# Kernel tuning notes

Hardware: AMD Instinct MI355X
Metric: run time of the kernel (lower is better)

## Reference

```python
import jax, jax.numpy as jnp
import numpy as np

B, S, H, NH, L = 8, 768, 768, 12, 12
W = 128          # one-sided window = attention_window // 2 (chunk_size=256)
D = H // NH      # head dim = 64
FF = 4 * H
EPS = 1e-12      # LongformerConfig layer_norm_eps
MAX_POS = 1024


def setup_inputs() -> dict:
    key = jax.random.key(0)
    ks = iter(jax.random.split(key, 64))
    rn = lambda shape, s=0.02: jax.random.normal(next(ks), shape, jnp.float32) * s
    inp = {
        "embedding": jax.random.normal(next(ks), (B, S, H), jnp.float32),
        "mask": jnp.ones((B, S), jnp.int32),  # unused by the original forward's core call
        "pos_emb": rn((MAX_POS, H)),
        "tte": rn((H,)),  # token_type embedding row 0 (token_type_ids are all zero)
        "emb_ln_g": jnp.ones((H,), jnp.float32),
        "emb_ln_b": jnp.zeros((H,), jnp.float32),
        "Wq": rn((L, H, H)), "bq": jnp.zeros((L, H), jnp.float32),
        "Wk": rn((L, H, H)), "bk": jnp.zeros((L, H), jnp.float32),
        "Wv": rn((L, H, H)), "bv": jnp.zeros((L, H), jnp.float32),
        "Wo": rn((L, H, H)), "bo": jnp.zeros((L, H), jnp.float32),
        "ln1_g": jnp.ones((L, H), jnp.float32), "ln1_b": jnp.zeros((L, H), jnp.float32),
        "Wi": rn((L, H, FF)), "bi": jnp.zeros((L, FF), jnp.float32),
        "Wo2": rn((L, FF, H)), "bo2": jnp.zeros((L, H), jnp.float32),
        "ln2_g": jnp.ones((L, H), jnp.float32), "ln2_b": jnp.zeros((L, H), jnp.float32),
        "gate_w": rn((H,)), "gate_b": jnp.zeros((), jnp.float32),
    }
    return inp


def layer_norm(x, g, b):
    mu = jnp.mean(x, axis=-1, keepdims=True)
    var = jnp.mean(jnp.square(x - mu), axis=-1, keepdims=True)
    return (x - mu) * jax.lax.rsqrt(var + EPS) * g + b


def sliding_window_attention(q, k, v):
    # q,k,v: [B,S,H]; each query attends to keys within +-W positions (band of 2W+1).
    n = S // W
    split = lambda x: x.reshape(B, S, NH, D).transpose(0, 2, 1, 3)  # [B,NH,S,D]
    qh = split(q) / np.sqrt(D)
    kh, vh = split(k), split(v)
    qc = qh.reshape(B, NH, n, W, D)

    def chunk3(x):
        # pad one chunk of zeros each side, gather [prev, cur, next] key chunks
        xp = jnp.pad(x, ((0, 0), (0, 0), (W, W), (0, 0))).reshape(B, NH, n + 2, W, D)
        return jnp.concatenate([xp[:, :, i:i + n] for i in range(3)], axis=3)  # [B,NH,n,3W,D]

    k3, v3 = chunk3(kh), chunk3(vh)
    scores = jnp.einsum('bhnqd,bhnkd->bhnqk', qc, k3)  # [B,NH,n,W,3W]

    qi = jnp.arange(W)[:, None]
    kj = jnp.arange(3 * W)[None, :]
    rel = kj - W - qi                                   # relative position j - i
    jglob = (jnp.arange(n)[:, None, None] - 1) * W + kj  # absolute key position
    valid = (jnp.abs(rel) <= W) & (jglob >= 0) & (jglob < S)  # [n,W,3W]

    scores = jnp.where(valid, scores, -1e9)
    p = jax.nn.softmax(scores, axis=-1)
    out = jnp.einsum('bhnqk,bhnkd->bhnqd', p, v3)
    return out.reshape(B, NH, S, D).transpose(0, 2, 1, 3).reshape(B, S, H)


def reference(embedding, mask, pos_emb, tte, emb_ln_g, emb_ln_b,
              Wq, bq, Wk, bk, Wv, bv, Wo, bo, ln1_g, ln1_b,
              Wi, bi, Wo2, bo2, ln2_g, ln2_b, gate_w, gate_b):
    # embeddings (position ids start at padding_idx+1 = 2, RoBERTa-style)
    pos_ids = jnp.arange(S) + 2
    x = embedding + pos_emb[pos_ids] + tte
    x = layer_norm(x, emb_ln_g, emb_ln_b)

    def layer(h, p):
        wq, b_q, wk, b_k, wv, b_v, wo, b_o, g1, be1, wi, b_i, wo2, b_o2, g2, be2 = p
        q = h @ wq + b_q
        k = h @ wk + b_k
        v = h @ wv + b_v
        a = sliding_window_attention(q, k, v)
        h = layer_norm(h + a @ wo + b_o, g1, be1)
        ff = jax.nn.gelu(h @ wi + b_i, approximate=False)
        h = layer_norm(h + ff @ wo2 + b_o2, g2, be2)
        return h, None

    x, _ = jax.lax.scan(layer, x, (Wq, bq, Wk, bk, Wv, bv, Wo, bo, ln1_g, ln1_b,
                                   Wi, bi, Wo2, bo2, ln2_g, ln2_b))
    gate = x @ gate_w + gate_b  # [B,S]
    return x, gate
```

## Files before the change

kernel.cpp:

```cpp
#include <hip/hip_runtime.h>
#include <hip/hip_bf16.h>
#include <math.h>
#include <stdint.h>

typedef __hip_bfloat16 bf16;
typedef __attribute__((ext_vector_type(8))) __bf16 bf16x8;
typedef __attribute__((ext_vector_type(4))) float f32x4;

#define HDIM 768
#define MROWS 6144
#define NCHUNK 6

__device__ __forceinline__ float bf2f(unsigned int u) {
  union { unsigned int i; float f; } c; c.i = u << 16; return c.f;
}

__device__ __forceinline__ void gload16(const void* g, void* l) {
  __builtin_amdgcn_global_load_lds((const __attribute__((address_space(1))) void*)g,
                                   (__attribute__((address_space(3))) void*)l, 16, 0, 0);
}

__device__ __forceinline__ float gelu_f(float v) {
  const float u2 = 1.5957691216057308f * (v + 0.044715f * v * v * v);
  const float e = __expf(u2);
  const float th = 1.f - 2.f / (e + 1.f);
  return 0.5f * v * (1.f + th);
}

__global__ __launch_bounds__(256) void wconv(
    const float* __restrict__ Wq, const float* __restrict__ Wk,
    const float* __restrict__ Wv, const float* __restrict__ Wo,
    const float* __restrict__ Wi, const float* __restrict__ Wo2,
    bf16* __restrict__ wt)
{
  __shared__ float tile[32][33];
  const int bid = blockIdx.x;
  const float* src; bf16* dst; int K, N, tIdx;
  if (bid < 2304) {
    int m = bid / 576; tIdx = bid % 576; K = 768; N = 768;
    src = (m == 0) ? Wq : (m == 1) ? Wk : (m == 2) ? Wv : Wo;
    dst = wt + (size_t)m * 589824;
  } else if (bid < 4608) {
    tIdx = bid - 2304; K = 768; N = 3072; src = Wi; dst = wt + 2359296;
  } else {
    tIdx = bid - 4608; K = 3072; N = 768; src = Wo2; dst = wt + 4718592;
  }
  const int tilesN = N >> 5;
  const int tn = tIdx % tilesN, tk = tIdx / tilesN;
  const int n0 = tn * 32, k0 = tk * 32;
  const int tx = threadIdx.x & 31, ty = threadIdx.x >> 5;
#pragma unroll
  for (int r = 0; r < 4; ++r)
    tile[ty + r * 8][tx] = src[(size_t)(k0 + ty + r * 8) * N + n0 + tx];
  __syncthreads();
#pragma unroll
  for (int r = 0; r < 4; ++r)
    dst[(size_t)(n0 + ty + r * 8) * K + k0 + tx] = __float2bfloat16(tile[tx][ty + r * 8]);
}

__global__ __launch_bounds__(512, 2) void gemm256(
    const bf16* __restrict__ A, const bf16* __restrict__ Bt,
    void* __restrict__ out, const float* __restrict__ b0,
    const float* __restrict__ b1, const float* __restrict__ b2,
    int gx, int N, int K, int NT, int epi)
{
  __shared__ __align__(16) bf16 As[2][2][8192];
  __shared__ __align__(16) bf16 Bs[2][2][8192];

  const int nwg = gridDim.x;
  const int wg = blockIdx.x;
  const int L = (wg & 7) * (nwg >> 3) + (wg >> 3);
  const int bx = L % gx, by = L / gx;
  const int m0 = by * 256, n0 = bx * 256;

  const int t = threadIdx.x;
  const int lane = t & 63;
  const int w = t >> 6;
  const int wr = w >> 2;
  const int wc = w & 3;
  const int fr = lane & 15;
  const int g = lane >> 4;

  f32x4 acc[8][4];
#pragma unroll
  for (int i = 0; i < 8; ++i)
#pragma unroll
    for (int j = 0; j < 4; ++j) acc[i][j] = (f32x4)0.f;

  const int r0 = t >> 2, q0 = t & 3;
  const int sq0 = q0 ^ ((r0 >> 1) & 3);
  const bf16* gA0 = A + (size_t)(m0 + r0) * K + sq0 * 8;
  const bf16* gB0 = Bt + (size_t)(n0 + r0) * K + sq0 * 8;
  const int dst0 = t * 16;

  unsigned offA[8], offB[4];
#pragma unroll
  for (int mf = 0; mf < 8; ++mf) {
    const int R = wr * 128 + mf * 16 + fr;
    offA[mf] = (unsigned)((R * 64 + g * 16) ^ (((R >> 1) & 3) << 4));
  }
#pragma unroll
  for (int nf = 0; nf < 4; ++nf) {
    const int R = wc * 64 + nf * 16 + fr;
    offB[nf] = (unsigned)((R * 64 + g * 16) ^ (((R >> 1) & 3) << 4));
  }
  const unsigned ldsA = (unsigned)(uintptr_t)&As[0][0][0];
  const unsigned ldsB = (unsigned)(uintptr_t)&Bs[0][0][0];

#define STAGE(KT, DB, KH) {                                                \
    const bf16* a_ = gA0 + (size_t)(KT) * 64 + (KH) * 32;                  \
    const bf16* b_ = gB0 + (size_t)(KT) * 64 + (KH) * 32;                  \
    gload16(a_, (char*)As[DB][KH] + dst0);                                 \
    gload16(a_ + (size_t)128 * K, (char*)As[DB][KH] + dst0 + 8192);        \
    gload16(b_, (char*)Bs[DB][KH] + dst0);                                 \
    gload16(b_ + (size_t)128 * K, (char*)Bs[DB][KH] + dst0 + 8192); }

  STAGE(0, 0, 0)
  STAGE(0, 0, 1)
  asm volatile("s_waitcnt vmcnt(4)" ::: "memory");
  __builtin_amdgcn_s_barrier();

#define PHASE(KT, KH, DB) {                                                \
    bf16x8 af[8], bfr[4];                                                  \
    const unsigned baA_ = ldsA + (DB) * 32768u + (KH) * 16384u;            \
    const unsigned baB_ = ldsB + (DB) * 32768u + (KH) * 16384u;            \
    _Pragma("unroll")                                                      \
    for (int mf = 0; mf < 8; ++mf)                                         \
      asm volatile("ds_read_b128 %0, %1" : "=v"(af[mf]) : "v"(baA_ + offA[mf])); \
    _Pragma("unroll")                                                      \
    for (int nf = 0; nf < 4; ++nf)                                         \
      asm volatile("ds_read_b128 %0, %1" : "=v"(bfr[nf]) : "v"(baB_ + offB[nf])); \
    const int pf_ = ((KT) + 1 < NT) ? (KT) + 1 : (KT);                     \
    STAGE(pf_, (DB) ^ 1, KH)                                               \
    asm volatile("s_waitcnt lgkmcnt(0)" ::: "memory");                     \
    __builtin_amdgcn_sched_barrier(0);                                     \
    __builtin_amdgcn_s_setprio(1);                                         \
    _Pragma("unroll")                                                      \
    for (int mf = 0; mf < 8; ++mf)                                         \
      _Pragma("unroll")                                                    \
      for (int nf = 0; nf < 4; ++nf)                                       \
        acc[mf][nf] = __builtin_amdgcn_mfma_f32_16x16x32_bf16(af[mf], bfr[nf], acc[mf][nf], 0, 0, 0); \
    __builtin_amdgcn_s_setprio(0);                                         \
    asm volatile("s_waitcnt vmcnt(4)" ::: "memory");                       \
    __builtin_amdgcn_s_barrier();                                          \
  }

#pragma unroll 1
  for (int kt = 0; kt < NT; kt += 2) {
    PHASE(kt, 0, 0)
    PHASE(kt, 1, 0)
    PHASE(kt + 1, 0, 1)
    PHASE(kt + 1, 1, 1)
  }
  asm volatile("s_waitcnt vmcnt(0)" ::: "memory");
#undef PHASE
#undef STAGE

  const int rr = (lane >> 4) * 4;
  const int cc0 = lane & 15;
  if (epi == 0) {
    const int mat = n0 / HDIM;
    const float* bias = (mat == 0) ? b0 : (mat == 1) ? b1 : b2;
    const float qs = (mat == 0) ? 0.125f : 1.0f;
    bf16* dst = (bf16*)out + (size_t)mat * MROWS * HDIM;
    const int nl = n0 - mat * HDIM;
#pragma unroll
    for (int mf = 0; mf < 8; ++mf)
#pragma unroll
      for (int nf = 0; nf < 4; ++nf) {
        const int row = m0 + wr * 128 + mf * 16 + rr;
        const int col = nl + wc * 64 + nf * 16 + cc0;
        const float bv = bias[col];
#pragma unroll
        for (int r = 0; r < 4; ++r)
          dst[(size_t)(row + r) * HDIM + col] = __float2bfloat16((acc[mf][nf][r] + bv) * qs);
      }
  } else if (epi == 2) {
    bf16* dst = (bf16*)out;
#pragma unroll
    for (int mf = 0; mf < 8; ++mf)
#pragma unroll
      for (int nf = 0; nf < 4; ++nf) {
        const int row = m0 + wr * 128 + mf * 16 + rr;
        const int col = n0 + wc * 64 + nf * 16 + cc0;
        const float bv = b0[col];
#pragma unroll
        for (int r = 0; r < 4; ++r)
          dst[(size_t)(row + r) * N + col] = __float2bfloat16(gelu_f(acc[mf][nf][r] + bv));
      }
  } else {
    float* dst = (float*)out;
#pragma unroll
    for (int mf = 0; mf < 8; ++mf)
#pragma unroll
      for (int nf = 0; nf < 4; ++nf) {
        const int row = m0 + wr * 128 + mf * 16 + rr;
        const int col = n0 + wc * 64 + nf * 16 + cc0;
        const float bv = b0[col];
#pragma unroll
        for (int r = 0; r < 4; ++r)
          dst[(size_t)(row + r) * N + col] = acc[mf][nf][r] + bv;
      }
  }
}

__global__ __launch_bounds__(256) void attn_mfma(
    const bf16* __restrict__ qkv, bf16* __restrict__ attb)
{
  const int c = blockIdx.x, h = blockIdx.y, b = blockIdx.z;
  __shared__ unsigned int Vtw[64 * 64];
  __shared__ __align__(16) bf16 Pl[4][32 * 40];
  const int t = threadIdx.x;
  const int lane = t & 63;
  const int w = t >> 6;
  const int fr = lane & 15;
  const int g = lane >> 4;
  const bf16* Km = qkv + (size_t)4718592;
  const bf16* Vm = qkv + (size_t)9437184;
  const size_t qrow0 = (size_t)(b * 768 + c * 128);

  bf16x8 qf[2][2];
#pragma unroll
  for (int nt = 0; nt < 2; ++nt)
#pragma unroll
    for (int ks = 0; ks < 2; ++ks)
      qf[nt][ks] = *(const bf16x8*)(qkv + (qrow0 + w * 32 + nt * 16 + fr) * HDIM + h * 64 + ks * 32 + g * 8);

  f32x4 oacc[4][2];
#pragma unroll
  for (int i = 0; i < 4; ++i) { oacc[i][0] = (f32x4)0.f; oacc[i][1] = (f32x4)0.f; }
  float mrun[2] = {-1e30f, -1e30f};
  float lrun[2] = {0.f, 0.f};

#pragma unroll 1
  for (int cc = c - 1; cc <= c + 1; ++cc) {
    if (cc < 0 || cc >= NCHUNK) continue;
    __syncthreads();
    {
      const int d0 = (t & 7) * 8;
#pragma unroll
      for (int half = 0; half < 2; ++half) {
        const int kp2 = (t >> 3) + half * 32;
        const bf16* vr = Vm + ((size_t)(b * 768 + cc * 128) + kp2 * 2) * HDIM + h * 64 + d0;
        uint4 r0 = *(const uint4*)vr;
        uint4 r1 = *(const uint4*)(vr + HDIM);
        unsigned int a0[4] = {r0.x, r0.y, r0.z, r0.w};
        unsigned int a1[4] = {r1.x, r1.y, r1.z, r1.w};
#pragma unroll
        for (int e = 0; e < 8; ++e) {
          const int d = d0 + e;
          unsigned int lo = (a0[e >> 1] >> ((e & 1) * 16)) & 0xffffu;
          unsigned int hi = (a1[e >> 1] >> ((e & 1) * 16)) & 0xffffu;
          unsigned int byteoff = (unsigned int)(d * 256 + kp2 * 4);
          byteoff ^= ((((d >> 3) ^ d) & 7) << 4);
          Vtw[byteoff >> 2] = lo | (hi << 16);
        }
      }
    }
    __syncthreads();
    const int mode = (cc < c) ? 0 : (cc == c ? 1 : 2);
    const bf16* Kc = Km + ((size_t)(b * 768 + cc * 128)) * HDIM + h * 64;

#pragma unroll 1
    for (int kb = 0; kb < 4; ++kb) {
      f32x4 sacc[2][2];
      sacc[0][0] = sacc[0][1] = sacc[1][0] = sacc[1][1] = (f32x4)0.f;
#pragma unroll
      for (int ks = 0; ks < 2; ++ks)
#pragma unroll
        for (int mt = 0; mt < 2; ++mt) {
          bf16x8 kf = *(const bf16x8*)(Kc + (size_t)(kb * 32 + mt * 16 + fr) * HDIM + ks * 32 + g * 8);
          sacc[mt][0] = __builtin_amdgcn_mfma_f32_16x16x32_bf16(kf, qf[0][ks], sacc[mt][0], 0, 0, 0);
          sacc[mt][1] = __builtin_amdgcn_mfma_f32_16x16x32_bf16(kf, qf[1][ks], sacc[mt][1], 0, 0, 0);
        }
#pragma unroll
      for (int nt = 0; nt < 2; ++nt) {
        const int iq = w * 32 + nt * 16 + fr;
        float pm = -1e30f;
#pragma unroll
        for (int mt = 0; mt < 2; ++mt)
#pragma unroll
          for (int r = 0; r < 4; ++r) {
            const int j = kb * 32 + mt * 16 + g * 4 + r;
            const bool valid = (mode == 1) || (mode == 0 ? (j >= iq) : (j <= iq));
            const float sv = valid ? sacc[mt][nt][r] : -1e30f;
            sacc[mt][nt][r] = sv;
            pm = fmaxf(pm, sv);
          }
        pm = fmaxf(pm, __shfl_xor(pm, 16));
        pm = fmaxf(pm, __shfl_xor(pm, 32));
        const float mnew = fmaxf(fmaxf(mrun[nt], pm), -1e20f);
        const float sc = __expf(mrun[nt] - mnew);
        mrun[nt] = mnew;
        lrun[nt] *= sc;
#pragma unroll
        for (int mt = 0; mt < 4; ++mt) oacc[mt][nt] *= sc;
        float ps = 0.f;
#pragma unroll
        for (int mt = 0; mt < 2; ++mt) {
          union { bf16 hh[4]; uint2 uu; } pk;
#pragma unroll
          for (int r = 0; r < 4; ++r) {
            const float p = __expf(sacc[mt][nt][r] - mnew);
            ps += p;
            pk.hh[r] = __float2bfloat16(p);
          }
          *(uint2*)(&Pl[w][(nt * 16 + fr) * 40 + mt * 16 + g * 4]) = pk.uu;
        }
        ps += __shfl_xor(ps, 16);
        ps += __shfl_xor(ps, 32);
        lrun[nt] += ps;
      }
      bf16x8 bpf[2];
#pragma unroll
      for (int nt = 0; nt < 2; ++nt)
        bpf[nt] = *(const bf16x8*)(&Pl[w][(nt * 16 + fr) * 40 + g * 8]);
#pragma unroll
      for (int mt = 0; mt < 4; ++mt) {
        const int d = mt * 16 + fr;
        unsigned int byteoff = (unsigned int)(d * 256 + kb * 64 + g * 16);
        byteoff ^= ((((d >> 3) ^ d) & 7) << 4);
        bf16x8 vf = *(const bf16x8*)((const char*)Vtw + byteoff);
        oacc[mt][0] = __builtin_amdgcn_mfma_f32_16x16x32_bf16(vf, bpf[0], oacc[mt][0], 0, 0, 0);
        oacc[mt][1] = __builtin_amdgcn_mfma_f32_16x16x32_bf16(vf, bpf[1], oacc[mt][1], 0, 0, 0);
      }
    }
  }
#pragma unroll
  for (int nt = 0; nt < 2; ++nt) {
    const float rl = 1.f / lrun[nt];
    bf16* orow = attb + (qrow0 + w * 32 + nt * 16 + fr) * HDIM + h * 64;
#pragma unroll
    for (int mt = 0; mt < 4; ++mt) {
      union { bf16 hh[4]; uint2 uu; } ok;
#pragma unroll
      for (int r = 0; r < 4; ++r) ok.hh[r] = __float2bfloat16(oacc[mt][nt][r] * rl);
      *(uint2*)(orow + mt * 16 + g * 4) = ok.uu;
    }
  }
}

__device__ __forceinline__ void blk_reduce2(float& s1, float& s2) {
#pragma unroll
  for (int o = 32; o > 0; o >>= 1) { s1 += __shfl_xor(s1, o); s2 += __shfl_xor(s2, o); }
  __shared__ float red[8];
  const int w = threadIdx.x >> 6;
  if ((threadIdx.x & 63) == 0) { red[w] = s1; red[4 + w] = s2; }
  __syncthreads();
  s1 = red[0] + red[1] + red[2] + red[3];
  s2 = red[4] + red[5] + red[6] + red[7];
}

__global__ __launch_bounds__(256) void embed_ln(
    const float* __restrict__ emb, const float* __restrict__ pos,
    const float* __restrict__ tte, const float* __restrict__ g,
    const float* __restrict__ bt, float* __restrict__ x, bf16* __restrict__ xb)
{
  const int row = blockIdx.x;
  const int s = row % 768;
  const int t = threadIdx.x;
  const size_t base = (size_t)row * HDIM;
  const size_t pbase = (size_t)(s + 2) * HDIM;
  float v[3];
#pragma unroll
  for (int i = 0; i < 3; ++i) {
    const int idx = t + i * 256;
    v[i] = emb[base + idx] + pos[pbase + idx] + tte[idx];
  }
  float s1 = v[0] + v[1] + v[2];
  float s2 = v[0]*v[0] + v[1]*v[1] + v[2]*v[2];
  blk_reduce2(s1, s2);
  const float mu = s1 * (1.f / 768.f);
  const float var = s2 * (1.f / 768.f) - mu * mu;
  const float inv = rsqrtf(var + 1e-12f);
#pragma unroll
  for (int i = 0; i < 3; ++i) {
    const int idx = t + i * 256;
    const float o = (v[i] - mu) * inv * g[idx] + bt[idx];
    x[base + idx] = o;
    xb[base + idx] = __float2bfloat16(o);
  }
}

__global__ __launch_bounds__(256) void add_ln(
    const float* __restrict__ tmp, float* __restrict__ x, bf16* __restrict__ xb,
    const float* __restrict__ g, const float* __restrict__ bt)
{
  const int row = blockIdx.x;
  const int t = threadIdx.x;
  const size_t base = (size_t)row * HDIM;
  float v[3];
#pragma unroll
  for (int i = 0; i < 3; ++i) {
    const int idx = t + i * 256;
    v[i] = x[base + idx] + tmp[base + idx];
  }
  float s1 = v[0] + v[1] + v[2];
  float s2 = v[0]*v[0] + v[1]*v[1] + v[2]*v[2];
  blk_reduce2(s1, s2);
  const float mu = s1 * (1.f / 768.f);
  const float var = s2 * (1.f / 768.f) - mu * mu;
  const float inv = rsqrtf(var + 1e-12f);
#pragma unroll
  for (int i = 0; i < 3; ++i) {
    const int idx = t + i * 256;
    const float o = (v[i] - mu) * inv * g[idx] + bt[idx];
    x[base + idx] = o;
    xb[base + idx] = __float2bfloat16(o);
  }
}

__global__ __launch_bounds__(256) void gate_kernel(
    const float* __restrict__ x, const float* __restrict__ gw,
    const float* __restrict__ gb, float* __restrict__ out)
{
  const int row = blockIdx.x * 4 + (threadIdx.x >> 6);
  const int lane = threadIdx.x & 63;
  const float* xr = x + (size_t)row * HDIM;
  float s = 0.f;
#pragma unroll
  for (int i = 0; i < 12; ++i) s += xr[lane + i * 64] * gw[lane + i * 64];
#pragma unroll
  for (int o = 32; o > 0; o >>= 1) s += __shfl_xor(s, o);
  if (lane == 0) out[row] = s + gb[0];
}

extern "C" void kernel_launch(void* const* d_in, const int* in_sizes, int n_in,
                              void* d_out, int out_size, void* d_ws, size_t ws_size,
                              hipStream_t stream)
{
  const float* emb = (const float*)d_in[0];
  const float* pos = (const float*)d_in[2];
  const float* tte = (const float*)d_in[3];
  const float* eg  = (const float*)d_in[4];
  const float* eb  = (const float*)d_in[5];
  const float* Wq  = (const float*)d_in[6];
  const float* bq  = (const float*)d_in[7];
  const float* Wk  = (const float*)d_in[8];
  const float* bk  = (const float*)d_in[9];
  const float* Wv  = (const float*)d_in[10];
  const float* bv  = (const float*)d_in[11];
  const float* Wo  = (const float*)d_in[12];
  const float* bo  = (const float*)d_in[13];
  const float* g1  = (const float*)d_in[14];
  const float* be1 = (const float*)d_in[15];
  const float* Wi  = (const float*)d_in[16];
  const float* bi  = (const float*)d_in[17];
  const float* Wo2 = (const float*)d_in[18];
  const float* bo2 = (const float*)d_in[19];
  const float* g2  = (const float*)d_in[20];
  const float* be2 = (const float*)d_in[21];
  const float* gw  = (const float*)d_in[22];
  const float* gb  = (const float*)d_in[23];

  char* wsp = (char*)d_ws;
  bf16* wt   = (bf16*)wsp;
  bf16* xb   = (bf16*)(wsp + 14155776);
  bf16* qkvb = (bf16*)(wsp + 23592960);
  float* tmp = (float*)(wsp + 61341696);
  bf16* attb = qkvb + (size_t)3 * 4718592;
  bf16* ffb  = qkvb;
  float* x   = (float*)d_out;
  float* gate = x + 4718592;

  embed_ln<<<6144, 256, 0, stream>>>(emb, pos, tte, eg, eb, x, xb);

  for (int l = 0; l < 12; ++l) {
    wconv<<<6912, 256, 0, stream>>>(Wq + (size_t)l * 589824, Wk + (size_t)l * 589824,
                                    Wv + (size_t)l * 589824, Wo + (size_t)l * 589824,
                                    Wi + (size_t)l * 2359296, Wo2 + (size_t)l * 2359296, wt);
    gemm256<<<216, 512, 0, stream>>>(xb, wt, qkvb,
        bq + l * 768, bk + l * 768, bv + l * 768, 9, 2304, 768, 12, 0);
    attn_mfma<<<dim3(6, 12, 8), 256, 0, stream>>>(qkvb, attb);
    gemm256<<<72, 512, 0, stream>>>(attb, wt + 1769472, tmp,
        bo + l * 768, nullptr, nullptr, 3, 768, 768, 12, 3);
    add_ln<<<6144, 256, 0, stream>>>(tmp, x, xb, g1 + l * 768, be1 + l * 768);
    gemm256<<<288, 512, 0, stream>>>(xb, wt + 2359296, ffb,
        bi + l * 3072, nullptr, nullptr, 12, 3072, 768, 12, 2);
    gemm256<<<72, 512, 0, stream>>>(ffb, wt + 4718592, tmp,
        bo2 + l * 768, nullptr, nullptr, 3, 768, 3072, 48, 3);
    add_ln<<<6144, 256, 0, stream>>>(tmp, x, xb, g2 + l * 768, be2 + l * 768);
  }

  gate_kernel<<<1536, 256, 0, stream>>>(x, gw, gb, gate);
}
```

Before: 3.218 ms.

## Shrink GEMM tiles to 256x128 with 3-stage pipeline and store residual outputs in bf16

```diff
diff --git a/kernel.cpp b/kernel.cpp
--- a/kernel.cpp
+++ b/kernel.cpp
@@ -58,26 +58,25 @@
     dst[(size_t)(n0 + ty + r * 8) * K + k0 + tx] = __float2bfloat16(tile[tx][ty + r * 8]);
 }
 
-__global__ __launch_bounds__(512, 2) void gemm256(
+__global__ __launch_bounds__(256, 2) void gemm_mn(
     const bf16* __restrict__ A, const bf16* __restrict__ Bt,
     void* __restrict__ out, const float* __restrict__ b0,
     const float* __restrict__ b1, const float* __restrict__ b2,
     int gx, int N, int K, int NT, int epi)
 {
-  __shared__ __align__(16) bf16 As[2][2][8192];
-  __shared__ __align__(16) bf16 Bs[2][2][8192];
+  __shared__ __align__(16) bf16 As[3][8192];
+  __shared__ __align__(16) bf16 Bs[3][4096];
 
   const int nwg = gridDim.x;
   const int wg = blockIdx.x;
   const int L = (wg & 7) * (nwg >> 3) + (wg >> 3);
   const int bx = L % gx, by = L / gx;
-  const int m0 = by * 256, n0 = bx * 256;
+  const int m0 = by * 256, n0 = bx * 128;
 
   const int t = threadIdx.x;
   const int lane = t & 63;
   const int w = t >> 6;
-  const int wr = w >> 2;
-  const int wc = w & 3;
+  const int wr = w >> 1, wc = w & 1;
   const int fr = lane & 15;
   const int g = lane >> 4;
 
@@ -87,10 +86,10 @@
 #pragma unroll
     for (int j = 0; j < 4; ++j) acc[i][j] = (f32x4)0.f;
 
-  const int r0 = t >> 2, q0 = t & 3;
-  const int sq0 = q0 ^ ((r0 >> 1) & 3);
-  const bf16* gA0 = A + (size_t)(m0 + r0) * K + sq0 * 8;
-  const bf16* gB0 = Bt + (size_t)(n0 + r0) * K + sq0 * 8;
+  const int rA = t >> 2, q0 = t & 3;
+  const int sq = q0 ^ ((rA >> 1) & 3);
+  const bf16* gA0 = A + (size_t)(m0 + rA) * K + sq * 8;
+  const bf16* gB0 = Bt + (size_t)(n0 + rA) * K + sq * 8;
   const int dst0 = t * 16;
 
   unsigned offA[8], offB[4];
@@ -104,36 +103,39 @@
     const int R = wc * 64 + nf * 16 + fr;
     offB[nf] = (unsigned)((R * 64 + g * 16) ^ (((R >> 1) & 3) << 4));
   }
-  const unsigned ldsA = (unsigned)(uintptr_t)&As[0][0][0];
-  const unsigned ldsB = (unsigned)(uintptr_t)&Bs[0][0][0];
-
-#define STAGE(KT, DB, KH) {                                                \
-    const bf16* a_ = gA0 + (size_t)(KT) * 64 + (KH) * 32;                  \
-    const bf16* b_ = gB0 + (size_t)(KT) * 64 + (KH) * 32;                  \
-    gload16(a_, (char*)As[DB][KH] + dst0);                                 \
-    gload16(a_ + (size_t)128 * K, (char*)As[DB][KH] + dst0 + 8192);        \
-    gload16(b_, (char*)Bs[DB][KH] + dst0);                                 \
-    gload16(b_ + (size_t)128 * K, (char*)Bs[DB][KH] + dst0 + 8192); }
-
-  STAGE(0, 0, 0)
-  STAGE(0, 0, 1)
-  asm volatile("s_waitcnt vmcnt(4)" ::: "memory");
-  __builtin_amdgcn_s_barrier();
-
-#define PHASE(KT, KH, DB) {                                                \
+  const unsigned ldsA = (unsigned)(uintptr_t)&As[0][0];
+  const unsigned ldsB = (unsigned)(uintptr_t)&Bs[0][0];
+
+#define STAGE(KT, RB) {                                                    \
+    const bf16* a_ = gA0 + (size_t)(KT) * 32;                              \
+    const bf16* b_ = gB0 + (size_t)(KT) * 32;                              \
+    gload16(a_,                    (char*)As[RB] + dst0);                  \
+    gload16(a_ + (size_t)64 * K,   (char*)As[RB] + dst0 + 4096);           \
+    gload16(a_ + (size_t)128 * K,  (char*)As[RB] + dst0 + 8192);           \
+    gload16(a_ + (size_t)192 * K,  (char*)As[RB] + dst0 + 12288);          \
+    gload16(b_,                    (char*)Bs[RB] + dst0);                  \
+    gload16(b_ + (size_t)64 * K,   (char*)Bs[RB] + dst0 + 4096); }
+
+  STAGE(0, 0)
+  STAGE(1, 1)
+
+#define ITER(KT, CUR, PFB) {                                               \
+    const int pf_ = ((KT) + 2 < NT) ? (KT) + 2 : NT - 1;                   \
+    STAGE(pf_, PFB)                                                        \
+    asm volatile("s_waitcnt vmcnt(12)" ::: "memory");                      \
+    __builtin_amdgcn_s_barrier();                                          \
     bf16x8 af[8], bfr[4];                                                  \
-    const unsigned baA_ = ldsA + (DB) * 32768u + (KH) * 16384u;            \
-    const unsigned baB_ = ldsB + (DB) * 32768u + (KH) * 16384u;            \
+    const unsigned baA_ = ldsA + (CUR) * 16384u;                           \
+    const unsigned baB_ = ldsB + (CUR) * 8192u;                            \
     _Pragma("unroll")                                                      \
     for (int mf = 0; mf < 8; ++mf)                                         \
       asm volatile("ds_read_b128 %0, %1" : "=v"(af[mf]) : "v"(baA_ + offA[mf])); \
     _Pragma("unroll")                                                      \
     for (int nf = 0; nf < 4; ++nf)                                         \
       asm volatile("ds_read_b128 %0, %1" : "=v"(bfr[nf]) : "v"(baB_ + offB[nf])); \
-    const int pf_ = ((KT) + 1 < NT) ? (KT) + 1 : (KT);                     \
-    STAGE(pf_, (DB) ^ 1, KH)                                               \
     asm volatile("s_waitcnt lgkmcnt(0)" ::: "memory");                     \
     __builtin_amdgcn_sched_barrier(0);                                     \
+    __builtin_amdgcn_s_barrier();                                          \
     __builtin_amdgcn_s_setprio(1);                                         \
     _Pragma("unroll")                                                      \
     for (int mf = 0; mf < 8; ++mf)                                         \
@@ -141,19 +143,16 @@
       for (int nf = 0; nf < 4; ++nf)                                       \
         acc[mf][nf] = __builtin_amdgcn_mfma_f32_16x16x32_bf16(af[mf], bfr[nf], acc[mf][nf], 0, 0, 0); \
     __builtin_amdgcn_s_setprio(0);                                         \
-    asm volatile("s_waitcnt vmcnt(4)" ::: "memory");                       \
-    __builtin_amdgcn_s_barrier();                                          \
   }
 
 #pragma unroll 1
-  for (int kt = 0; kt < NT; kt += 2) {
-    PHASE(kt, 0, 0)
-    PHASE(kt, 1, 0)
-    PHASE(kt + 1, 0, 1)
-    PHASE(kt + 1, 1, 1)
+  for (int kt = 0; kt < NT; kt += 3) {
+    ITER(kt, 0, 2)
+    ITER(kt + 1, 1, 0)
+    ITER(kt + 2, 2, 1)
   }
   asm volatile("s_waitcnt vmcnt(0)" ::: "memory");
-#undef PHASE
+#undef ITER
 #undef STAGE
 
   const int rr = (lane >> 4) * 4;
@@ -189,7 +188,7 @@
           dst[(size_t)(row + r) * N + col] = __float2bfloat16(gelu_f(acc[mf][nf][r] + bv));
       }
   } else {
-    float* dst = (float*)out;
+    bf16* dst = (bf16*)out;
 #pragma unroll
     for (int mf = 0; mf < 8; ++mf)
 #pragma unroll
@@ -199,7 +198,7 @@
         const float bv = b0[col];
 #pragma unroll
         for (int r = 0; r < 4; ++r)
-          dst[(size_t)(row + r) * N + col] = acc[mf][nf][r] + bv;
+          dst[(size_t)(row + r) * N + col] = __float2bfloat16(acc[mf][nf][r] + bv);
       }
   }
 }
@@ -383,7 +382,7 @@
 }
 
 __global__ __launch_bounds__(256) void add_ln(
-    const float* __restrict__ tmp, float* __restrict__ x, bf16* __restrict__ xb,
+    const bf16* __restrict__ tmp, float* __restrict__ x, bf16* __restrict__ xb,
     const float* __restrict__ g, const float* __restrict__ bt)
 {
   const int row = blockIdx.x;
@@ -393,7 +392,7 @@
 #pragma unroll
   for (int i = 0; i < 3; ++i) {
     const int idx = t + i * 256;
-    v[i] = x[base + idx] + tmp[base + idx];
+    v[i] = x[base + idx] + __bfloat162float(tmp[base + idx]);
   }
   float s1 = v[0] + v[1] + v[2];
   float s2 = v[0]*v[0] + v[1]*v[1] + v[2]*v[2];
@@ -457,7 +456,7 @@
   bf16* wt   = (bf16*)wsp;
   bf16* xb   = (bf16*)(wsp + 14155776);
   bf16* qkvb = (bf16*)(wsp + 23592960);
-  float* tmp = (float*)(wsp + 61341696);
+  bf16* tmp  = (bf16*)(wsp + 61341696);
   bf16* attb = qkvb + (size_t)3 * 4718592;
   bf16* ffb  = qkvb;
   float* x   = (float*)d_out;
@@ -469,16 +468,16 @@
     wconv<<<6912, 256, 0, stream>>>(Wq + (size_t)l * 589824, Wk + (size_t)l * 589824,
                                     Wv + (size_t)l * 589824, Wo + (size_t)l * 589824,
                                     Wi + (size_t)l * 2359296, Wo2 + (size_t)l * 2359296, wt);
-    gemm256<<<216, 512, 0, stream>>>(xb, wt, qkvb,
-        bq + l * 768, bk + l * 768, bv + l * 768, 9, 2304, 768, 12, 0);
+    gemm_mn<<<432, 256, 0, stream>>>(xb, wt, qkvb,
+        bq + l * 768, bk + l * 768, bv + l * 768, 18, 2304, 768, 24, 0);
     attn_mfma<<<dim3(6, 12, 8), 256, 0, stream>>>(qkvb, attb);
-    gemm256<<<72, 512, 0, stream>>>(attb, wt + 1769472, tmp,
-        bo + l * 768, nullptr, nullptr, 3, 768, 768, 12, 3);
+    gemm_mn<<<144, 256, 0, stream>>>(attb, wt + 1769472, tmp,
+        bo + l * 768, nullptr, nullptr, 6, 768, 768, 24, 3);
     add_ln<<<6144, 256, 0, stream>>>(tmp, x, xb, g1 + l * 768, be1 + l * 768);
-    gemm256<<<288, 512, 0, stream>>>(xb, wt + 2359296, ffb,
-        bi + l * 3072, nullptr, nullptr, 12, 3072, 768, 12, 2);
-    gemm256<<<72, 512, 0, stream>>>(ffb, wt + 4718592, tmp,
-        bo2 + l * 768, nullptr, nullptr, 3, 768, 3072, 48, 3);
+    gemm_mn<<<576, 256, 0, stream>>>(xb, wt + 2359296, ffb,
+        bi + l * 3072, nullptr, nullptr, 24, 3072, 768, 24, 2);
+    gemm_mn<<<144, 256, 0, stream>>>(ffb, wt + 4718592, tmp,
+        bo2 + l * 768, nullptr, nullptr, 6, 768, 3072, 96, 3);
     add_ln<<<6144, 256, 0, stream>>>(tmp, x, xb, g2 + l * 768, be2 + l * 768);
   }
 
```

Result: faster. 2.848 ms (-11.5%).
